# Kernel tuning notes

Hardware: AMD Instinct MI355X
Metric: run time of the kernel (lower is better)

Reference implementation:

```python
import jax, jax.numpy as jnp
import numpy as np

D_MODEL = 1024
NUM_HEADS = 16
D_K = D_MODEL // NUM_HEADS
D_FF = 4096
LN_EPS = 1e-5


def layernorm(x, gamma, beta):
    mu = jnp.mean(x, axis=-1, keepdims=True)
    var = jnp.mean(jnp.square(x - mu), axis=-1, keepdims=True)
    return (x - mu) * jax.lax.rsqrt(var + LN_EPS) * gamma + beta


def setup_inputs() -> dict:
    key = jax.random.key(0)
    ks = jax.random.split(key, 16)
    s = 1.0 / np.sqrt(D_MODEL)
    sf = 1.0 / np.sqrt(D_FF)
    inp = {
        "x": jax.random.normal(ks[0], (2, 2048, D_MODEL), dtype=jnp.float32),
        # attention sublayer LN
        "ln1_g": jnp.ones((D_MODEL,), jnp.float32),
        "ln1_b": jnp.zeros((D_MODEL,), jnp.float32),
        # QKV / output projections, stored as [in, out]
        "Wq": jax.random.uniform(ks[1], (D_MODEL, D_MODEL), jnp.float32, -s, s),
        "bq": jax.random.uniform(ks[2], (D_MODEL,), jnp.float32, -s, s),
        "Wk": jax.random.uniform(ks[3], (D_MODEL, D_MODEL), jnp.float32, -s, s),
        "bk": jax.random.uniform(ks[4], (D_MODEL,), jnp.float32, -s, s),
        "Wv": jax.random.uniform(ks[5], (D_MODEL, D_MODEL), jnp.float32, -s, s),
        "bv": jax.random.uniform(ks[6], (D_MODEL,), jnp.float32, -s, s),
        "Wo": jax.random.uniform(ks[7], (D_MODEL, D_MODEL), jnp.float32, -s, s),
        "bo": jax.random.uniform(ks[8], (D_MODEL,), jnp.float32, -s, s),
        # FFN sublayer LN
        "ln2_g": jnp.ones((D_MODEL,), jnp.float32),
        "ln2_b": jnp.zeros((D_MODEL,), jnp.float32),
        "W1": jax.random.uniform(ks[9], (D_MODEL, D_FF), jnp.float32, -s, s),
        "b1": jax.random.uniform(ks[10], (D_FF,), jnp.float32, -s, s),
        "W2": jax.random.uniform(ks[11], (D_FF, D_MODEL), jnp.float32, -sf, sf),
        "b2": jax.random.uniform(ks[12], (D_MODEL,), jnp.float32, -sf, sf),
    }
    return inp


def block_fwd(x, ln1_g, ln1_b, Wq, bq, Wk, bk, Wv, bv, Wo, bo,
              ln2_g, ln2_b, W1, b1, W2, b2):
    B, S, D = x.shape
    # --- attention sublayer (pre-LN + residual) ---
    h = layernorm(x, ln1_g, ln1_b)
    q = (h @ Wq + bq).reshape(B, S, NUM_HEADS, D_K)
    k = (h @ Wk + bk).reshape(B, S, NUM_HEADS, D_K)
    v = (h @ Wv + bv).reshape(B, S, NUM_HEADS, D_K)
    scale = 1.0 / np.sqrt(D_K)  # == sqrt(d_k)/d_k in source
    attn = jnp.einsum("bqhd,bkhd->bhqk", q, k) * scale  # [B,H,S,S]
    causal = jnp.arange(S)[:, None] >= jnp.arange(S)[None, :]
    attn = jnp.where(causal, attn, -jnp.inf)
    score = jax.nn.softmax(attn, axis=-1)
    o = jnp.einsum("bhqk,bkhd->bqhd", score, v).reshape(B, S, D)
    x = x + (o @ Wo + bo)
    # --- FFN sublayer (pre-LN + residual) ---
    h = layernorm(x, ln2_g, ln2_b)
    h = jax.nn.gelu(h @ W1 + b1, approximate=False)  # torch nn.GELU = exact erf
    return x + (h @ W2 + b2)


def reference(x, ln1_g, ln1_b, Wq, bq, Wk, bk, Wv, bv, Wo, bo,
              ln2_g, ln2_b, W1, b1, W2, b2):
    return block_fwd(x, ln1_g, ln1_b, Wq, bq, Wk, bk, Wv, bv, Wo, bo,
                     ln2_g, ln2_b, W1, b1, W2, b2)
```

## Files before the change

kernel.cpp:

```cpp
#include <hip/hip_runtime.h>
#include <hip/hip_bf16.h>
#include <hip/hip_fp8.h>
#include <math.h>

typedef unsigned short u16;
typedef unsigned char u8;
typedef unsigned int u32;
typedef long i64;
typedef __bf16 bf16x8 __attribute__((ext_vector_type(8)));
typedef float f32x4 __attribute__((ext_vector_type(4)));
typedef i64 i64x2 __attribute__((ext_vector_type(2)));

#define MFMA16(a, b, c) __builtin_amdgcn_mfma_f32_16x16x32_bf16(a, b, c, 0, 0, 0)
#define MFMA8(a, b, c) __builtin_amdgcn_mfma_f32_16x16x32_fp8_fp8(a, b, c, 0, 0, 0)

__device__ __forceinline__ u16 f2b(float f) {
    __bf16 h = (__bf16)f;
    return __builtin_bit_cast(u16, h);
}

__device__ __forceinline__ u8 f2f8(float f) {
    __hip_fp8_e4m3 h(f);
    return h.__x;
}

__device__ __forceinline__ void gld16(const void* g, void* l) {
    __builtin_amdgcn_global_load_lds(
        (const __attribute__((address_space(1))) unsigned int*)g,
        (__attribute__((address_space(3))) unsigned int*)l, 16, 0, 0);
}


__global__ __launch_bounds__(256) void transpose_all(
    const float* __restrict__ Wq, const float* __restrict__ Wk,
    const float* __restrict__ Wv, const float* __restrict__ Wo,
    const float* __restrict__ W1, const float* __restrict__ W2, u16* __restrict__ wqkvT,
    u16* __restrict__ woT, u16* __restrict__ w1T, u8* __restrict__ w2T8) {
    __shared__ float tile[32][33];
    int t = blockIdx.x;
    const float* in;
    u16* out = nullptr;
    int R, C;
    bool isf8 = false;
    if (t < 3072) {
        int m = t >> 10;
        t &= 1023;
        in = m == 0 ? Wq : (m == 1 ? Wk : Wv);
        out = wqkvT + m * 1048576;
        R = 1024; C = 1024;
    } else if (t < 4096) {
        t -= 3072; in = Wo; out = woT; R = 1024; C = 1024;
    } else if (t < 8192) {
        t -= 4096; in = W1; out = w1T; R = 1024; C = 4096;
    } else {
        t -= 8192; in = W2; R = 4096; C = 1024; isf8 = true;
    }
    int tilesX = C >> 5;
    int c0 = (t % tilesX) * 32, r0 = (t / tilesX) * 32;
    int tx = threadIdx.x, ty = threadIdx.y;
#pragma unroll
    for (int i = 0; i < 4; i++)
        tile[ty + i * 8][tx] = in[(size_t)(r0 + ty + i * 8) * C + c0 + tx];
    __syncthreads();
    if (isf8) {
        int pos = (r0 & ~63) + (tx >> 3) * 16 + ((r0 >> 5) & 1) * 8 + (tx & 7);
#pragma unroll
        for (int i = 0; i < 4; i++)
            w2T8[(size_t)(c0 + ty + i * 8) * 4096 + pos] = f2f8(tile[tx][ty + i * 8] * 64.0f);
    } else {
#pragma unroll
        for (int i = 0; i < 4; i++)
            out[(size_t)(c0 + ty + i * 8) * R + r0 + tx] = f2b(tile[tx][ty + i * 8]);
    }
}

__global__ __launch_bounds__(256) void ln_kernel(const float* __restrict__ x,
                                                 const float* __restrict__ g,
                                                 const float* __restrict__ b,
                                                 u16* __restrict__ out) {
    int row = blockIdx.x;
    int tid = threadIdx.x;
    const float* xr = x + (size_t)row * 1024;
    float4 v = ((const float4*)xr)[tid];
    float s = v.x + v.y + v.z + v.w;
    float s2 = v.x * v.x + v.y * v.y + v.z * v.z + v.w * v.w;
#pragma unroll
    for (int off = 32; off > 0; off >>= 1) {
        s += __shfl_xor(s, off);
        s2 += __shfl_xor(s2, off);
    }
    __shared__ float ps[4], ps2[4];
    int wid = tid >> 6;
    if ((tid & 63) == 0) { ps[wid] = s; ps2[wid] = s2; }
    __syncthreads();
    s = ps[0] + ps[1] + ps[2] + ps[3];
    s2 = ps2[0] + ps2[1] + ps2[2] + ps2[3];
    float mu = s * (1.0f / 1024.0f);
    float var = s2 * (1.0f / 1024.0f) - mu * mu;
    float rs = rsqrtf(var + 1e-5f);
    int c = tid * 4;
    ushort4 o;
    o.x = f2b((v.x - mu) * rs * g[c + 0] + b[c + 0]);
    o.y = f2b((v.y - mu) * rs * g[c + 1] + b[c + 1]);
    o.z = f2b((v.z - mu) * rs * g[c + 2] + b[c + 2]);
    o.w = f2b((v.w - mu) * rs * g[c + 3] + b[c + 3]);
    ((ushort4*)(out + (size_t)row * 1024))[tid] = o;
}

__global__ __launch_bounds__(256) void vtrans_kernel(const u16* __restrict__ Vb,
                                                     u16* __restrict__ VbT) {
    __shared__ u16 t[64][66];
    const int tid = threadIdx.x;
    const int s0 = blockIdx.x * 64;
    const int bh = blockIdx.y;
    const u16* src = Vb + (size_t)bh * 2048 * 64;
    u16* dst = VbT + (size_t)bh * 64 * 2048;
#pragma unroll
    for (int p = 0; p < 2; p++) {
        int idx = p * 256 + tid;
        int r = idx >> 3, dc = (idx & 7) * 8;
        uint4 v = *(const uint4*)&src[(size_t)(s0 + r) * 64 + dc];
        const u16* pv = (const u16*)&v;
#pragma unroll
        for (int j = 0; j < 8; j++) t[r][dc + j] = pv[j];
    }
    __syncthreads();
    int d = tid >> 2, sc = (tid & 3) * 16;
    u16 buf[16];
#pragma unroll
    for (int m = 0; m < 16; m++) {
        int cp = sc + m;
        int blk = cp >> 5, c = cp & 31;
        int srcw = blk * 32 + (c >> 1) + (c & 1) * 16;
        buf[m] = t[srcw][d];
    }
    *(uint4*)&dst[(size_t)d * 2048 + s0 + sc] = *(uint4*)&buf[0];
    *(uint4*)&dst[(size_t)d * 2048 + s0 + sc + 8] = *(uint4*)&buf[8];
}

#define EPI_QKV 0
#define EPI_RESID 1
#define EPI_GELU 2

__device__ __forceinline__ void gemm_stage(const u16* __restrict__ A,
                                           const u16* __restrict__ BT,
                                           u16 (&Asb)[128][32], u16 (&Bsb)[128][32],
                                           int m0, int n0, int K, int k0, int sr, int sdc,
                                           int wb) {
    gld16(&A[(size_t)(m0 + sr) * K + k0 + sdc], &Asb[0][0] + wb);
    gld16(&A[(size_t)(m0 + 64 + sr) * K + k0 + sdc], &Asb[0][0] + 2048 + wb);
    gld16(&BT[(size_t)(n0 + sr) * K + k0 + sdc], &Bsb[0][0] + wb);
    gld16(&BT[(size_t)(n0 + 64 + sr) * K + k0 + sdc], &Bsb[0][0] + 2048 + wb);
}

__device__ __forceinline__ void gemm_compute(const u16 (&Asb)[128][32],
                                             const u16 (&Bsb)[128][32], f32x4 (&acc)[4][4],
                                             int wm, int wn, int quad, int c15) {
    bf16x8 af[4], bfr[4];
#pragma unroll
    for (int i = 0; i < 4; i++) af[i] = *(const bf16x8*)&Asb[wm + i * 16 + c15][quad * 8];
#pragma unroll
    for (int j = 0; j < 4; j++) bfr[j] = *(const bf16x8*)&Bsb[wn + j * 16 + c15][quad * 8];
#pragma unroll
    for (int i = 0; i < 4; i++)
#pragma unroll
        for (int j = 0; j < 4; j++) acc[i][j] = MFMA16(af[i], bfr[j], acc[i][j]);
}

template <int EPI>
__global__ __launch_bounds__(256) void gemm_kernel(const u16* __restrict__ A,
                                                   const u16* __restrict__ BT,
                                                   const float* __restrict__ bias0,
                                                   const float* __restrict__ bias1,
                                                   const float* __restrict__ bias2,
                                                   void* __restrict__ outp,
                                                   const float* __restrict__ resid,
                                                   int N, int K) {
    __shared__ __align__(16) u16 As0[128][32], Bs0[128][32];
    __shared__ __align__(16) u16 As1[128][32], Bs1[128][32];
    const int tid = threadIdx.x;
    const int m0 = blockIdx.y * 128, n0 = blockIdx.x * 128;
    const int w = tid >> 6, lid = tid & 63, quad = lid >> 4, c15 = lid & 15;
    const int wm = (w >> 1) * 64, wn = (w & 1) * 64;
    const int sr = tid >> 2, sdc = (tid & 3) * 8;
    const int wb = (tid & 192) * 8;

    f32x4 acc[4][4] = {};

    gemm_stage(A, BT, As0, Bs0, m0, n0, K, 0, sr, sdc, wb);
    const int KT = K >> 5;
    for (int kt = 0; kt < KT; kt += 2) {
        __syncthreads();
        gemm_stage(A, BT, As1, Bs1, m0, n0, K, (kt + 1) << 5, sr, sdc, wb);
        gemm_compute(As0, Bs0, acc, wm, wn, quad, c15);
        __syncthreads();
        if (kt + 2 < KT) gemm_stage(A, BT, As0, Bs0, m0, n0, K, (kt + 2) << 5, sr, sdc, wb);
        gemm_compute(As1, Bs1, acc, wm, wn, quad, c15);
    }

    const int which = n0 >> 10;
    const float* bias = (EPI == EPI_QKV) ? (which == 0 ? bias0 : (which == 1 ? bias1 : bias2))
                                         : bias0;
    u16* qkv_dst = (u16*)outp + (size_t)which * 4194304;

#pragma unroll
    for (int i = 0; i < 4; i++) {
#pragma unroll
        for (int j = 0; j < 4; j++) {
#pragma unroll
            for (int r = 0; r < 4; r++) {
                int gr = m0 + wm + i * 16 + quad * 4 + r;
                int gc = n0 + wn + j * 16 + c15;
                if (EPI == EPI_QKV) {
                    int lc = gc & 1023;
                    float v = acc[i][j][r] + bias[lc];
                    int bb = gr >> 11, ss = gr & 2047, hh = lc >> 6, dd = lc & 63;
                    qkv_dst[((size_t)((bb * 16 + hh) * 2048 + ss)) * 64 + dd] = f2b(v);
                } else if (EPI == EPI_RESID) {
                    float v = acc[i][j][r] + bias[gc];
                    ((float*)outp)[(size_t)gr * N + gc] = resid[(size_t)gr * N + gc] + v;
                } else {
                    float v = acc[i][j][r] + bias[gc];
                    float u = v * (0.79788456f + 0.03567741f * v * v);
                    float e = __expf(2.0f * u);
                    float th = 1.0f - 2.0f / (e + 1.0f);
                    int g = gc & 63;
                    int pos = (gc & ~63) + ((g >> 3) & 3) * 16 + (g >> 5) * 8 + (g & 7);
                    ((u8*)outp)[(size_t)gr * N + pos] = f2f8(0.5f * v * (1.0f + th));
                }
            }
        }
    }
}

__global__ __launch_bounds__(256) void gemm64_kernel(const u16* __restrict__ A,
                                                     const u16* __restrict__ BT,
                                                     const float* __restrict__ bias,
                                                     float* __restrict__ outp,
                                                     const float* __restrict__ resid,
                                                     int N, int K) {
    __shared__ __align__(16) u16 As0[128][32], Bs0[64][32];
    __shared__ __align__(16) u16 As1[128][32], Bs1[64][32];
    const int tid = threadIdx.x;
    const int m0 = blockIdx.y * 128, n0 = blockIdx.x * 64;
    const int w = tid >> 6, lid = tid & 63, quad = lid >> 4, c15 = lid & 15;
    const int wm = (w >> 1) * 64, wn = (w & 1) * 32;
    const int sr = tid >> 2, sdc = (tid & 3) * 8;
    const int wb = (tid & 192) * 8;

    f32x4 acc[4][2] = {};

    auto stage = [&](u16 (&Asb)[128][32], u16 (&Bsb)[64][32], int k0) {
        gld16(&A[(size_t)(m0 + sr) * K + k0 + sdc], &Asb[0][0] + wb);
        gld16(&A[(size_t)(m0 + 64 + sr) * K + k0 + sdc], &Asb[0][0] + 2048 + wb);
        gld16(&BT[(size_t)(n0 + sr) * K + k0 + sdc], &Bsb[0][0] + wb);
    };
    auto compute = [&](const u16 (&Asb)[128][32], const u16 (&Bsb)[64][32]) {
        bf16x8 af[4], bfr[2];
#pragma unroll
        for (int i = 0; i < 4; i++) af[i] = *(const bf16x8*)&Asb[wm + i * 16 + c15][quad * 8];
#pragma unroll
        for (int j = 0; j < 2; j++) bfr[j] = *(const bf16x8*)&Bsb[wn + j * 16 + c15][quad * 8];
#pragma unroll
        for (int i = 0; i < 4; i++)
#pragma unroll
            for (int j = 0; j < 2; j++) acc[i][j] = MFMA16(af[i], bfr[j], acc[i][j]);
    };

    stage(As0, Bs0, 0);
    const int KT = K >> 5;
    for (int kt = 0; kt < KT; kt += 2) {
        __syncthreads();
        stage(As1, Bs1, (kt + 1) << 5);
        compute(As0, Bs0);
        __syncthreads();
        if (kt + 2 < KT) stage(As0, Bs0, (kt + 2) << 5);
        compute(As1, Bs1);
    }

#pragma unroll
    for (int i = 0; i < 4; i++) {
#pragma unroll
        for (int j = 0; j < 2; j++) {
#pragma unroll
            for (int r = 0; r < 4; r++) {
                int gr = m0 + wm + i * 16 + quad * 4 + r;
                int gc = n0 + wn + j * 16 + c15;
                float v = acc[i][j][r] + bias[gc];
                outp[(size_t)gr * N + gc] = resid[(size_t)gr * N + gc] + v;
            }
        }
    }
}

__global__ __launch_bounds__(256) void gemm_fp8_kernel(const u8* __restrict__ A,
                                                       const u8* __restrict__ BT,
                                                       const float* __restrict__ bias,
                                                       float* __restrict__ outp,
                                                       const float* __restrict__ resid,
                                                       int N, int K) {
    __shared__ __align__(16) u8 As0[128][64], Bs0[64][64];
    __shared__ __align__(16) u8 As1[128][64], Bs1[64][64];
    const int tid = threadIdx.x;
    const int m0 = blockIdx.y * 128, n0 = blockIdx.x * 64;
    const int w = tid >> 6, lid = tid & 63, quad = lid >> 4, c15 = lid & 15;
    const int wm = (w >> 1) * 64, wn = (w & 1) * 32;
    const int sr = tid >> 2, sdc = (tid & 3) * 16;
    const int wbB = (tid & 192) * 16;

    f32x4 acc[4][2] = {};

    auto stage = [&](u8 (&Asb)[128][64], u8 (&Bsb)[64][64], int k0) {
        gld16(&A[(size_t)(m0 + sr) * K + k0 + sdc], &Asb[0][0] + wbB);
        gld16(&A[(size_t)(m0 + 64 + sr) * K + k0 + sdc], &Asb[0][0] + 4096 + wbB);
        gld16(&BT[(size_t)(n0 + sr) * K + k0 + sdc], &Bsb[0][0] + wbB);
    };
    auto compute = [&](const u8 (&Asb)[128][64], const u8 (&Bsb)[64][64]) {
        i64x2 af[4], bfr[2];
#pragma unroll
        for (int i = 0; i < 4; i++)
            af[i] = *(const i64x2*)&Asb[wm + i * 16 + c15][quad * 16];
#pragma unroll
        for (int j = 0; j < 2; j++)
            bfr[j] = *(const i64x2*)&Bsb[wn + j * 16 + c15][quad * 16];
#pragma unroll
        for (int s = 0; s < 2; s++)
#pragma unroll
            for (int i = 0; i < 4; i++)
#pragma unroll
                for (int j = 0; j < 2; j++)
                    acc[i][j] = MFMA8(af[i][s], bfr[j][s], acc[i][j]);
    };

    stage(As0, Bs0, 0);
    const int KT = K >> 6;
    for (int kt = 0; kt < KT; kt += 2) {
        __syncthreads();
        stage(As1, Bs1, (kt + 1) << 6);
        compute(As0, Bs0);
        __syncthreads();
        if (kt + 2 < KT) stage(As0, Bs0, (kt + 2) << 6);
        compute(As1, Bs1);
    }

#pragma unroll
    for (int i = 0; i < 4; i++) {
#pragma unroll
        for (int j = 0; j < 2; j++) {
#pragma unroll
            for (int r = 0; r < 4; r++) {
                int gr = m0 + wm + i * 16 + quad * 4 + r;
                int gc = n0 + wn + j * 16 + c15;
                float v = acc[i][j][r] * (1.0f / 64.0f) + bias[gc];
                outp[(size_t)gr * N + gc] = resid[(size_t)gr * N + gc] + v;
            }
        }
    }
}

__device__ __forceinline__ void attn_step(const u16 (&KB)[2][64][32],
                                          const u16 (&VB)[2][64][32],
                                          u16 (&Psw)[2][16][48], const bf16x8 (&aq)[2],
                                          f32x4 (&o)[4], float (&lsum)[4], int kv0,
                                          int qr0, int quad, int c15) {
    bf16x8 bk[4][2];
#pragma unroll
    for (int nf = 0; nf < 4; nf++)
#pragma unroll
        for (int kd = 0; kd < 2; kd++)
            bk[nf][kd] = *(const bf16x8*)&KB[kd][nf * 16 + c15][quad * 8];
    f32x4 sf[4];
#pragma unroll
    for (int nf = 0; nf < 4; nf++) {
        f32x4 s = {};
        s = MFMA16(aq[0], bk[nf][0], s);
        s = MFMA16(aq[1], bk[nf][1], s);
        sf[nf] = s;
    }
    const bool domask = (kv0 + 63 > qr0);
    if (domask) {
#pragma unroll
        for (int r = 0; r < 4; r++) {
            int rowg = qr0 + quad * 4 + r;
#pragma unroll
            for (int nf = 0; nf < 4; nf++) {
                float p = (kv0 + nf * 16 + c15 <= rowg) ? __expf(sf[nf][r] * 0.125f) : 0.0f;
                sf[nf][r] = p;
                lsum[r] += p;
            }
        }
    } else {
#pragma unroll
        for (int r = 0; r < 4; r++)
#pragma unroll
            for (int nf = 0; nf < 4; nf++) {
                float p = __expf(sf[nf][r] * 0.125f);
                sf[nf][r] = p;
                lsum[r] += p;
            }
    }
#pragma unroll
    for (int ks = 0; ks < 2; ks++)
#pragma unroll
        for (int r = 0; r < 4; r++) {
            u32 pk = (u32)f2b(sf[2 * ks][r]) | ((u32)f2b(sf[2 * ks + 1][r]) << 16);
            *(u32*)&Psw[ks][quad * 4 + r][2 * c15] = pk;
        }
    asm volatile("s_waitcnt lgkmcnt(0)" ::: "memory");
    bf16x8 ap[2];
#pragma unroll
    for (int ks = 0; ks < 2; ks++) ap[ks] = *(const bf16x8*)&Psw[ks][c15][quad * 8];
#pragma unroll
    for (int df = 0; df < 4; df++) {
        bf16x8 bv0 = *(const bf16x8*)&VB[0][df * 16 + c15][quad * 8];
        bf16x8 bv1 = *(const bf16x8*)&VB[1][df * 16 + c15][quad * 8];
        o[df] = MFMA16(ap[0], bv0, o[df]);
        o[df] = MFMA16(ap[1], bv1, o[df]);
    }
}

__global__ __launch_bounds__(256) void attn_kernel(const u16* __restrict__ Q,
                                                   const u16* __restrict__ Kb,
                                                   const u16* __restrict__ VbT,
                                                   u16* __restrict__ attO) {
    __shared__ __align__(16) u16 Ks[2][2][64][32];
    __shared__ __align__(16) u16 Vs[2][2][64][32];
    __shared__ __align__(16) u16 Ps[4][2][16][48];

    const int tid = threadIdx.x;
    const int bh = blockIdx.x;
    const int qt = 31 - blockIdx.y;
    const int q0 = qt * 64;
    const size_t base = (size_t)bh * 2048 * 64;
    const u16* Qp = Q + base;
    const u16* Kp = Kb + base;
    const u16* Vp = VbT + (size_t)bh * 64 * 2048;
    const int w = tid >> 6, lane = tid & 63, quad = lane >> 4, c15 = lane & 15;
    const int qr0 = q0 + w * 16;
    const int sr = tid >> 2, sdc = (tid & 3) * 8;
    const int wb = (tid & 192) * 8;
    const int bb = bh >> 4, hh = bh & 15;

#define ATTN_STAGE(bi, kvo)                                                             \
    do {                                                                                \
        gld16(&Kp[(size_t)((kvo) + sr) * 64 + sdc], &Ks[bi][0][0][0] + wb);             \
        gld16(&Kp[(size_t)((kvo) + sr) * 64 + 32 + sdc], &Ks[bi][0][0][0] + 2048 + wb); \
        gld16(&Vp[(size_t)sr * 2048 + (kvo) + sdc], &Vs[bi][0][0][0] + wb);             \
        gld16(&Vp[(size_t)sr * 2048 + (kvo) + 32 + sdc], &Vs[bi][0][0][0] + 2048 + wb); \
    } while (0)

    bf16x8 aq[2];
#pragma unroll
    for (int ks = 0; ks < 2; ks++)
        aq[ks] = *(const bf16x8*)&Qp[(size_t)(qr0 + c15) * 64 + ks * 32 + quad * 8];

    f32x4 o[4] = {};
    float lsum[4] = {};
    const int steps = qt + 1;

    ATTN_STAGE(0, 0);
    for (int s = 0; s < steps; s++) {
        __syncthreads();
        if (s + 1 < steps) ATTN_STAGE((s + 1) & 1, (s + 1) << 6);
        attn_step(Ks[s & 1], Vs[s & 1], Ps[w], aq, o, lsum, s << 6, qr0, quad, c15);
    }

#pragma unroll
    for (int r = 0; r < 4; r++) {
        float l = lsum[r];
#pragma unroll
        for (int off = 1; off < 16; off <<= 1) l += __shfl_xor(l, off);
        float inv = 1.0f / l;
        int sg = qr0 + quad * 4 + r;
        size_t rowoff = ((size_t)(bb * 2048 + sg)) * 1024 + hh * 64;
#pragma unroll
        for (int df = 0; df < 4; df++) attO[rowoff + df * 16 + c15] = f2b(o[df][r] * inv);
    }
#undef ATTN_STAGE
}

extern "C" void kernel_launch(void* const* d_in, const int* in_sizes, int n_in,
                              void* d_out, int out_size, void* d_ws, size_t ws_size,
                              hipStream_t stream) {
    const float* x = (const float*)d_in[0];
    const float* ln1g = (const float*)d_in[1];
    const float* ln1b = (const float*)d_in[2];
    const float* Wq = (const float*)d_in[3];
    const float* bq = (const float*)d_in[4];
    const float* Wk = (const float*)d_in[5];
    const float* bk = (const float*)d_in[6];
    const float* Wv = (const float*)d_in[7];
    const float* bv = (const float*)d_in[8];
    const float* Wo = (const float*)d_in[9];
    const float* bo = (const float*)d_in[10];
    const float* ln2g = (const float*)d_in[11];
    const float* ln2b = (const float*)d_in[12];
    const float* W1 = (const float*)d_in[13];
    const float* b1 = (const float*)d_in[14];
    const float* W2 = (const float*)d_in[15];
    const float* b2 = (const float*)d_in[16];
    float* out = (float*)d_out;

    char* ws = (char*)d_ws;
    u16* wqkvT = (u16*)(ws + 0);
    u16* woT = (u16*)(ws + 6291456);
    u16* w1T = (u16*)(ws + 8388608);
    u8* w2T8 = (u8*)(ws + 16777216);
    u16* h = (u16*)(ws + 25165824);
    float* x1 = (float*)(ws + 33554432);
    u16* Qb = (u16*)(ws + 50331648);
    u16* Kb = (u16*)(ws + 58720256);
    u16* Vb = (u16*)(ws + 67108864);
    u16* VbT = (u16*)(ws + 75497472);
    u16* aO = Vb;
    u8* mid8 = (u8*)(ws + 50331648);

    transpose_all<<<12288, dim3(32, 8), 0, stream>>>(Wq, Wk, Wv, Wo, W1, W2, wqkvT, woT,
                                                     w1T, w2T8);

    ln_kernel<<<4096, 256, 0, stream>>>(x, ln1g, ln1b, h);

    gemm_kernel<EPI_QKV><<<dim3(24, 32), 256, 0, stream>>>(h, wqkvT, bq, bk, bv, Qb, nullptr,
                                                           3072, 1024);

    vtrans_kernel<<<dim3(32, 32), 256, 0, stream>>>(Vb, VbT);

    attn_kernel<<<dim3(32, 32), 256, 0, stream>>>(Qb, Kb, VbT, aO);

    gemm64_kernel<<<dim3(16, 32), 256, 0, stream>>>(aO, woT, bo, x1, x, 1024, 1024);

    ln_kernel<<<4096, 256, 0, stream>>>(x1, ln2g, ln2b, h);

    gemm_kernel<EPI_GELU><<<dim3(32, 32), 256, 0, stream>>>(h, w1T, b1, nullptr, nullptr, mid8,
                                                            nullptr, 4096, 1024);
    gemm_fp8_kernel<<<dim3(16, 32), 256, 0, stream>>>(mid8, w2T8, b2, out, x1, 1024, 4096);
}
```

Measured before the change: 323.1 us.

## Fuse V transpose into QKV GEMM epilogue and pack FP8 conversions

```diff
diff --git a/kernel.cpp b/kernel.cpp
--- a/kernel.cpp
+++ b/kernel.cpp
@@ -19,9 +19,10 @@
     return __builtin_bit_cast(u16, h);
 }
 
-__device__ __forceinline__ u8 f2f8(float f) {
-    __hip_fp8_e4m3 h(f);
-    return h.__x;
+__device__ __forceinline__ u32 cvt2fp8(float a, float b) {
+    u32 d;
+    asm("v_cvt_pk_fp8_f32 %0, %1, %2" : "=v"(d) : "v"(a), "v"(b));
+    return d;
 }
 
 __device__ __forceinline__ void gld16(const void* g, void* l) {
@@ -64,9 +65,12 @@
     __syncthreads();
     if (isf8) {
         int pos = (r0 & ~63) + (tx >> 3) * 16 + ((r0 >> 5) & 1) * 8 + (tx & 7);
-#pragma unroll
-        for (int i = 0; i < 4; i++)
-            w2T8[(size_t)(c0 + ty + i * 8) * 4096 + pos] = f2f8(tile[tx][ty + i * 8] * 64.0f);
+        u32 p01 = cvt2fp8(tile[tx][ty] * 64.0f, tile[tx][ty + 8] * 64.0f);
+        u32 p23 = cvt2fp8(tile[tx][ty + 16] * 64.0f, tile[tx][ty + 24] * 64.0f);
+        w2T8[(size_t)(c0 + ty) * 4096 + pos] = (u8)p01;
+        w2T8[(size_t)(c0 + ty + 8) * 4096 + pos] = (u8)(p01 >> 8);
+        w2T8[(size_t)(c0 + ty + 16) * 4096 + pos] = (u8)p23;
+        w2T8[(size_t)(c0 + ty + 24) * 4096 + pos] = (u8)(p23 >> 8);
     } else {
 #pragma unroll
         for (int i = 0; i < 4; i++)
@@ -107,37 +111,6 @@
     ((ushort4*)(out + (size_t)row * 1024))[tid] = o;
 }
 
-__global__ __launch_bounds__(256) void vtrans_kernel(const u16* __restrict__ Vb,
-                                                     u16* __restrict__ VbT) {
-    __shared__ u16 t[64][66];
-    const int tid = threadIdx.x;
-    const int s0 = blockIdx.x * 64;
-    const int bh = blockIdx.y;
-    const u16* src = Vb + (size_t)bh * 2048 * 64;
-    u16* dst = VbT + (size_t)bh * 64 * 2048;
-#pragma unroll
-    for (int p = 0; p < 2; p++) {
-        int idx = p * 256 + tid;
-        int r = idx >> 3, dc = (idx & 7) * 8;
-        uint4 v = *(const uint4*)&src[(size_t)(s0 + r) * 64 + dc];
-        const u16* pv = (const u16*)&v;
-#pragma unroll
-        for (int j = 0; j < 8; j++) t[r][dc + j] = pv[j];
-    }
-    __syncthreads();
-    int d = tid >> 2, sc = (tid & 3) * 16;
-    u16 buf[16];
-#pragma unroll
-    for (int m = 0; m < 16; m++) {
-        int cp = sc + m;
-        int blk = cp >> 5, c = cp & 31;
-        int srcw = blk * 32 + (c >> 1) + (c & 1) * 16;
-        buf[m] = t[srcw][d];
-    }
-    *(uint4*)&dst[(size_t)d * 2048 + s0 + sc] = *(uint4*)&buf[0];
-    *(uint4*)&dst[(size_t)d * 2048 + s0 + sc + 8] = *(uint4*)&buf[8];
-}
-
 #define EPI_QKV 0
 #define EPI_RESID 1
 #define EPI_GELU 2
@@ -155,16 +128,24 @@
 
 __device__ __forceinline__ void gemm_compute(const u16 (&Asb)[128][32],
                                              const u16 (&Bsb)[128][32], f32x4 (&acc)[4][4],
-                                             int wm, int wn, int quad, int c15) {
+                                             int wm, int wn, int quad, int c15,
+                                             bool swapV) {
     bf16x8 af[4], bfr[4];
 #pragma unroll
     for (int i = 0; i < 4; i++) af[i] = *(const bf16x8*)&Asb[wm + i * 16 + c15][quad * 8];
 #pragma unroll
     for (int j = 0; j < 4; j++) bfr[j] = *(const bf16x8*)&Bsb[wn + j * 16 + c15][quad * 8];
-#pragma unroll
-    for (int i = 0; i < 4; i++)
-#pragma unroll
-        for (int j = 0; j < 4; j++) acc[i][j] = MFMA16(af[i], bfr[j], acc[i][j]);
+    if (!swapV) {
+#pragma unroll
+        for (int i = 0; i < 4; i++)
+#pragma unroll
+            for (int j = 0; j < 4; j++) acc[i][j] = MFMA16(af[i], bfr[j], acc[i][j]);
+    } else {
+#pragma unroll
+        for (int i = 0; i < 4; i++)
+#pragma unroll
+            for (int j = 0; j < 4; j++) acc[i][j] = MFMA16(bfr[i], af[j], acc[i][j]);
+    }
 }
 
 template <int EPI>
@@ -184,6 +165,7 @@
     const int wm = (w >> 1) * 64, wn = (w & 1) * 64;
     const int sr = tid >> 2, sdc = (tid & 3) * 8;
     const int wb = (tid & 192) * 8;
+    const bool swapV = (EPI == EPI_QKV) && (n0 >= 2048);
 
     f32x4 acc[4][4] = {};
 
@@ -192,41 +174,87 @@
     for (int kt = 0; kt < KT; kt += 2) {
         __syncthreads();
         gemm_stage(A, BT, As1, Bs1, m0, n0, K, (kt + 1) << 5, sr, sdc, wb);
-        gemm_compute(As0, Bs0, acc, wm, wn, quad, c15);
+        gemm_compute(As0, Bs0, acc, wm, wn, quad, c15, swapV);
         __syncthreads();
         if (kt + 2 < KT) gemm_stage(A, BT, As0, Bs0, m0, n0, K, (kt + 2) << 5, sr, sdc, wb);
-        gemm_compute(As1, Bs1, acc, wm, wn, quad, c15);
+        gemm_compute(As1, Bs1, acc, wm, wn, quad, c15, swapV);
     }
 
     const int which = n0 >> 10;
     const float* bias = (EPI == EPI_QKV) ? (which == 0 ? bias0 : (which == 1 ? bias1 : bias2))
                                          : bias0;
-    u16* qkv_dst = (u16*)outp + (size_t)which * 4194304;
+
+    if (EPI == EPI_QKV && swapV) {
+        u16* vbt = (u16*)outp + (size_t)3 * 4194304;
+#pragma unroll
+        for (int i = 0; i < 4; i++) {
+#pragma unroll
+            for (int j = 0; j < 4; j++) {
+                int sg = m0 + wm + j * 16 + c15;
+                int bbq = sg >> 11, ss = sg & 2047;
+                int col = (ss & ~31) + (ss & 15) * 2 + ((ss >> 4) & 1);
+#pragma unroll
+                for (int r = 0; r < 4; r++) {
+                    int dg = (n0 - 2048) + wn + i * 16 + quad * 4 + r;
+                    float v = acc[i][j][r] + bias[dg];
+                    int hh = dg >> 6, dd = dg & 63;
+                    vbt[(((size_t)(bbq * 16 + hh) * 64 + dd) << 11) + col] = f2b(v);
+                }
+            }
+        }
+        return;
+    }
+
+    int posj[4];
+    if (EPI == EPI_GELU) {
+#pragma unroll
+        for (int j = 0; j < 4; j++) {
+            int gc = n0 + wn + j * 16 + c15;
+            int g = gc & 63;
+            posj[j] = (gc & ~63) + ((g >> 3) & 3) * 16 + ((g >> 5) & 1) * 8 + (g & 7);
+        }
+    }
 
 #pragma unroll
     for (int i = 0; i < 4; i++) {
 #pragma unroll
         for (int j = 0; j < 4; j++) {
-#pragma unroll
-            for (int r = 0; r < 4; r++) {
-                int gr = m0 + wm + i * 16 + quad * 4 + r;
+            if (EPI == EPI_GELU) {
                 int gc = n0 + wn + j * 16 + c15;
-                if (EPI == EPI_QKV) {
-                    int lc = gc & 1023;
-                    float v = acc[i][j][r] + bias[lc];
-                    int bb = gr >> 11, ss = gr & 2047, hh = lc >> 6, dd = lc & 63;
-                    qkv_dst[((size_t)((bb * 16 + hh) * 2048 + ss)) * 64 + dd] = f2b(v);
-                } else if (EPI == EPI_RESID) {
+                float vv[4];
+#pragma unroll
+                for (int r = 0; r < 4; r++) {
                     float v = acc[i][j][r] + bias[gc];
-                    ((float*)outp)[(size_t)gr * N + gc] = resid[(size_t)gr * N + gc] + v;
-                } else {
-                    float v = acc[i][j][r] + bias[gc];
-                    float u = v * (0.79788456f + 0.03567741f * v * v);
-                    float e = __expf(2.0f * u);
-                    float th = 1.0f - 2.0f / (e + 1.0f);
-                    int g = gc & 63;
-                    int pos = (gc & ~63) + ((g >> 3) & 3) * 16 + (g >> 5) * 8 + (g & 7);
-                    ((u8*)outp)[(size_t)gr * N + pos] = f2f8(0.5f * v * (1.0f + th));
+                    float t = v * v;
+                    float u2 = v * (1.59576912f + 0.07135482f * t);
+                    float e = __expf(u2);
+                    float q = __frcp_rn(e + 1.0f);
+                    vv[r] = v - v * q;
+                }
+                u32 p01 = cvt2fp8(vv[0], vv[1]);
+                u32 p23 = cvt2fp8(vv[2], vv[3]);
+                int gr = m0 + wm + i * 16 + quad * 4;
+                u8* dst = (u8*)outp + (size_t)gr * N + posj[j];
+                dst[0] = (u8)p01;
+                dst[N] = (u8)(p01 >> 8);
+                dst[2 * N] = (u8)p23;
+                dst[3 * N] = (u8)(p23 >> 8);
+            } else {
+#pragma unroll
+                for (int r = 0; r < 4; r++) {
+                    int gr = m0 + wm + i * 16 + quad * 4 + r;
+                    int gc = n0 + wn + j * 16 + c15;
+                    if (EPI == EPI_QKV) {
+                        int lc = gc & 1023;
+                        float v = acc[i][j][r] + bias[lc];
+                        int bb = gr >> 11, ss = gr & 2047, hh = lc >> 6, dd = lc & 63;
+                        u16* qkv_dst = (u16*)outp + (size_t)which * 4194304;
+                        qkv_dst[((size_t)((bb * 16 + hh) * 2048 + ss)) * 64 + dd] = f2b(v);
+                    } else {
+                        float v = acc[i][j][r] + bias[gc];
+                        ((float*)outp)[(size_t)gr * N + gc] =
+                            resid[(size_t)gr * N + gc] + v;
+                    }
                 }
             }
         }
@@ -510,9 +538,8 @@
     float* x1 = (float*)(ws + 33554432);
     u16* Qb = (u16*)(ws + 50331648);
     u16* Kb = (u16*)(ws + 58720256);
-    u16* Vb = (u16*)(ws + 67108864);
+    u16* aO = (u16*)(ws + 67108864);
     u16* VbT = (u16*)(ws + 75497472);
-    u16* aO = Vb;
     u8* mid8 = (u8*)(ws + 50331648);
 
     transpose_all<<<12288, dim3(32, 8), 0, stream>>>(Wq, Wk, Wv, Wo, W1, W2, wqkvT, woT,
@@ -522,8 +549,6 @@
 
     gemm_kernel<EPI_QKV><<<dim3(24, 32), 256, 0, stream>>>(h, wqkvT, bq, bk, bv, Qb, nullptr,
                                                            3072, 1024);
-
-    vtrans_kernel<<<dim3(32, 32), 256, 0, stream>>>(Vb, VbT);
 
     attn_kernel<<<dim3(32, 32), 256, 0, stream>>>(Qb, Kb, VbT, aO);
 
```

Result: slower. 340.0 us (+5.2%).
